# Kernel optimization log

Hardware: AMD Instinct MI355X
Metric: run time of the kernel (lower is better)

Reference implementation:

```python
import jax, jax.numpy as jnp
import numpy as np

B, N, D = 8, 512, 1024
E, H, TOP_K = 8, 8, 2
HD = D // H
EPS = 1e-5


def setup_inputs() -> dict:
    key = jax.random.key(0)
    ks = jax.random.split(key, 8)
    # kaiming_uniform with a=sqrt(5) over fan_in=N -> bound = sqrt(6/((1+5)*N)) = 1/sqrt(N)
    bound_w = 1.0 / np.sqrt(N)
    bound_lin = 1.0 / np.sqrt(D)
    return {
        "x": jax.random.normal(ks[0], (B, N, D), dtype=jnp.float32),
        "weight": jax.random.uniform(ks[1], (E, H, N, N), jnp.float32, -bound_w, bound_w),
        "bias": jnp.zeros((E, H, N), jnp.float32),
        "router_w": jax.random.uniform(ks[2], (E, D), jnp.float32, -bound_lin, bound_lin),
        "in_w": jax.random.uniform(ks[3], (D, D), jnp.float32, -bound_lin, bound_lin),
        "in_b": jax.random.uniform(ks[4], (D,), jnp.float32, -bound_lin, bound_lin),
        "out_w": jax.random.uniform(ks[5], (D, D), jnp.float32, -bound_lin, bound_lin),
        "out_b": jax.random.uniform(ks[6], (D,), jnp.float32, -bound_lin, bound_lin),
    }


def reference(x, weight, bias, router_w, in_w, in_b, out_w, out_b):
    # Router: mean-pool tokens, linear, softmax, top-k
    router_logits = x.mean(axis=1) @ router_w.T              # (B, E)
    router_probs = jax.nn.softmax(router_logits, axis=-1)
    top_w, top_i = jax.lax.top_k(router_probs, TOP_K)        # (B, K)
    top_w = top_w / top_w.sum(axis=-1, keepdims=True)

    # Input projection -> (B, H, hd, N), layer-norm over token axis N (no affine)
    xp = x @ in_w.T + in_b                                   # (B, N, D)
    xr = xp.reshape(B, N, H, HD).transpose(0, 2, 3, 1)       # (B, H, hd, N)
    mu = xr.mean(axis=-1, keepdims=True)
    var = xr.var(axis=-1, keepdims=True)
    xn = (xr - mu) * jax.lax.rsqrt(var + EPS)

    # Gather per-(batch, head, k) NxN expert matrices, row-softmax
    w = weight[top_i].transpose(0, 2, 1, 3, 4)               # (B, H, K, N, N)
    b = bias[top_i].transpose(0, 2, 1, 3)                    # (B, H, K, N)
    w_attn = jax.nn.softmax(w, axis=-1)

    # out[b,h,k,d,m] = sum_n xn[b,h,d,n] * w_attn[b,h,k,m,n]
    out = jnp.einsum('bhdn,bhkmn->bhkdm', xn, w_attn)
    out = out + b[:, :, :, None, :]                          # (B, H, K, hd, N)
    out = (out * top_w[:, None, :, None, None]).sum(axis=2)  # (B, H, hd, N)

    out = out.transpose(0, 3, 1, 2).reshape(B, N, D)         # (B, N, D)
    out = out @ out_w.T + out_b

    # Load-balancing aux loss
    top1 = top_i[:, 0]
    expert_mask = jax.nn.one_hot(top1, E, dtype=jnp.float32)
    aux = E * (router_probs.mean(axis=0) * expert_mask.mean(axis=0)).sum()
    return out, aux
```

## Files before the change

### kernel.cpp

```cpp
#include <hip/hip_runtime.h>
#include <hip/hip_bf16.h>

#define Bv 8
#define Nv 512
#define Dv 1024
#define Ev 8
#define Hv 8
#define HDv 128
#define EPSv 1e-5f

typedef __attribute__((ext_vector_type(8))) short short8;
typedef __attribute__((ext_vector_type(4))) float f32x4;

__device__ __forceinline__ unsigned short f2b(float f) {
    __hip_bfloat16 h = __float2bfloat16(f);
    return *reinterpret_cast<unsigned short*>(&h);
}
__device__ __forceinline__ float bf2f(unsigned int u) {
    union { unsigned int i; float f; } v; v.i = u << 16; return v.f;
}
__device__ __forceinline__ unsigned int blend2(unsigned int a, unsigned int b,
                                               float tw0, float tw1) {
    float lo = tw0 * bf2f(a & 0xffffu) + tw1 * bf2f(b & 0xffffu);
    float hi = tw0 * bf2f(a >> 16)     + tw1 * bf2f(b >> 16);
    return (unsigned int)f2b(lo) | ((unsigned int)f2b(hi) << 16);
}

__device__ __forceinline__ void gld16(const void* g, void* l) {
    __builtin_amdgcn_global_load_lds(
        (const __attribute__((address_space(1))) void*)(uintptr_t)(g),
        (__attribute__((address_space(3))) void*)(uintptr_t)(l), 16, 0, 0);
}

__global__ __launch_bounds__(256) void k_pre(const float* __restrict__ x,
                                             const float* __restrict__ weight,
                                             const float* __restrict__ w1,
                                             const float* __restrict__ w2,
                                             unsigned short* __restrict__ xb,
                                             float* __restrict__ part_x,
                                             unsigned short* __restrict__ wa,
                                             unsigned short* __restrict__ w1b,
                                             unsigned short* __restrict__ w2b) {
    int bid = blockIdx.x;
    int t = threadIdx.x;
    if (bid < 128) {
        int b = bid >> 4, c = bid & 15;
        const float* px = x + ((size_t)b * Nv + c * 32) * Dv + t * 4;
        unsigned short* qx = xb + ((size_t)b * Nv + c * 32) * Dv + t * 4;
        float4 s4 = make_float4(0.f, 0.f, 0.f, 0.f);
        #pragma unroll 8
        for (int r = 0; r < 32; ++r) {
            float4 v = *(const float4*)(px + (size_t)r * Dv);
            s4.x += v.x; s4.y += v.y; s4.z += v.z; s4.w += v.w;
            uint2 pk;
            pk.x = (unsigned)f2b(v.x) | ((unsigned)f2b(v.y) << 16);
            pk.y = (unsigned)f2b(v.z) | ((unsigned)f2b(v.w) << 16);
            *(uint2*)(qx + (size_t)r * Dv) = pk;
        }
        *(float4*)(part_x + ((size_t)(b * 16 + c)) * Dv + t * 4) = s4;
        return;
    }
    if (bid < 1152) {
        int lane = t & 63;
        int r0 = ((bid - 128) * 4 + (t >> 6)) * 8;
        const float* wp = weight + (size_t)r0 * Nv + lane * 4;
        float v[8][8];
        #pragma unroll
        for (int r = 0; r < 8; ++r) {
            float4 a = *(const float4*)(wp + (size_t)r * Nv);
            float4 b = *(const float4*)(wp + (size_t)r * Nv + 256);
            v[r][0] = a.x; v[r][1] = a.y; v[r][2] = a.z; v[r][3] = a.w;
            v[r][4] = b.x; v[r][5] = b.y; v[r][6] = b.z; v[r][7] = b.w;
        }
        float sm[8];
        #pragma unroll
        for (int r = 0; r < 8; ++r) {
            #pragma unroll
            for (int i = 0; i < 8; ++i) v[r][i] = __expf(v[r][i]);
            float s01 = v[r][0] + v[r][1], s23 = v[r][2] + v[r][3];
            float s45 = v[r][4] + v[r][5], s67 = v[r][6] + v[r][7];
            sm[r] = (s01 + s23) + (s45 + s67);
        }
        for (int off = 1; off < 64; off <<= 1) {
            #pragma unroll
            for (int r = 0; r < 8; ++r) sm[r] += __shfl_xor(sm[r], off);
        }
        unsigned short* wq = wa + (size_t)r0 * Nv + lane * 4;
        #pragma unroll
        for (int r = 0; r < 8; ++r) {
            float inv = 1.f / sm[r];
            uint2 p0, p1;
            p0.x = (unsigned)f2b(v[r][0] * inv) | ((unsigned)f2b(v[r][1] * inv) << 16);
            p0.y = (unsigned)f2b(v[r][2] * inv) | ((unsigned)f2b(v[r][3] * inv) << 16);
            p1.x = (unsigned)f2b(v[r][4] * inv) | ((unsigned)f2b(v[r][5] * inv) << 16);
            p1.y = (unsigned)f2b(v[r][6] * inv) | ((unsigned)f2b(v[r][7] * inv) << 16);
            *(uint2*)(wq + (size_t)r * Nv) = p0;
            *(uint2*)(wq + (size_t)r * Nv + 256) = p1;
        }
        return;
    }
    int base = (bid - 1152) * 2048;
    const float* src; unsigned short* dst;
    if (base < 1048576) { src = w1; dst = w1b; }
    else                { src = w2; dst = w2b; base -= 1048576; }
    float4 a = *(const float4*)(src + base + t * 4);
    float4 b = *(const float4*)(src + base + 1024 + t * 4);
    uint2 p0, p1;
    p0.x = (unsigned)f2b(a.x) | ((unsigned)f2b(a.y) << 16);
    p0.y = (unsigned)f2b(a.z) | ((unsigned)f2b(a.w) << 16);
    p1.x = (unsigned)f2b(b.x) | ((unsigned)f2b(b.y) << 16);
    p1.y = (unsigned)f2b(b.z) | ((unsigned)f2b(b.w) << 16);
    *(uint2*)(dst + base + t * 4) = p0;
    *(uint2*)(dst + base + 1024 + t * 4) = p1;
}

template <int MODE>
__global__ __launch_bounds__(256) void k_gemm(
    const unsigned short* __restrict__ A,
    const unsigned short* __restrict__ W,
    const float* __restrict__ bias,
    void* __restrict__ Cv,
    float2* __restrict__ part,
    const float* __restrict__ part_x,
    float* __restrict__ xmean,
    int M, int Nn, int K) {
    __shared__ __align__(16) unsigned short sA[3][128 * 64];
    __shared__ __align__(16) unsigned short sB[3][128 * 64];
    const int t = threadIdx.x;
    const int bn = blockIdx.x * 128;
    const int bm = blockIdx.y * 128;
    const int lane = t & 63;
    const int w = t >> 6, wm = w >> 1, wn = w & 1;
    const int fr = lane & 15, fq = lane >> 4;
    const int NT = K >> 6;
    f32x4 acc[4][4] = {};

#define STAGE(s, k0)                                                        \
    {                                                                       \
        _Pragma("unroll")                                                   \
        for (int i_ = 0; i_ < 4; ++i_) {                                    \
            int c_ = t + i_ * 256;                                          \
            int row_ = c_ >> 3, col_ = c_ & 7;                              \
            int cs_ = col_ ^ (row_ & 7);                                    \
            gld16(A + (size_t)(bm + row_) * K + (k0) + cs_ * 8, &sA[s][c_ * 8]); \
            gld16(W + (size_t)(bn + row_) * K + (k0) + cs_ * 8, &sB[s][c_ * 8]); \
        }                                                                   \
    }

    STAGE(0, 0);
    STAGE(1, 64);
    if (MODE == 2) {
        int blk = blockIdx.y * 8 + blockIdx.x;
        int o = blk * 32 + (t >> 3);
        int c2 = t & 7;
        int b2 = o >> 10, d2 = o & 1023;
        float S = part_x[((size_t)(b2 * 16 + c2)) * Dv + d2]
                + part_x[((size_t)(b2 * 16 + c2 + 8)) * Dv + d2];
        S += __shfl_xor(S, 1); S += __shfl_xor(S, 2); S += __shfl_xor(S, 4);
        if (c2 == 0) xmean[o] = S * (1.f / Nv);
    }
    for (int it = 0; it < NT; ++it) {
        if (it + 2 < NT) {
            STAGE((it + 2) % 3, (it + 2) * 64);
            asm volatile("s_waitcnt vmcnt(16)" ::: "memory");
        } else if (it + 1 < NT) {
            asm volatile("s_waitcnt vmcnt(8)" ::: "memory");
        } else {
            asm volatile("s_waitcnt vmcnt(0)" ::: "memory");
        }
        __builtin_amdgcn_s_barrier();
        const unsigned short* pA = sA[it % 3];
        const unsigned short* pB = sB[it % 3];
        #pragma unroll
        for (int kk = 0; kk < 2; ++kk) {
            short8 af[4], bv[4];
            #pragma unroll
            for (int i = 0; i < 4; ++i)
                af[i] = *(const short8*)&pA[(wm * 64 + i * 16 + fr) * 64 + (((kk << 2) + fq) ^ (fr & 7)) * 8];
            #pragma unroll
            for (int j = 0; j < 4; ++j)
                bv[j] = *(const short8*)&pB[(wn * 64 + j * 16 + fr) * 64 + (((kk << 2) + fq) ^ (fr & 7)) * 8];
            #pragma unroll
            for (int i = 0; i < 4; ++i)
                #pragma unroll
                for (int j = 0; j < 4; ++j)
                    acc[i][j] = __builtin_amdgcn_mfma_f32_16x16x32_bf16(af[i], bv[j], acc[i][j], 0, 0, 0);
        }
        __builtin_amdgcn_s_barrier();
    }
#undef STAGE
    if (MODE == 0) {
        #pragma unroll
        for (int j = 0; j < 4; ++j) {
            const int n = bn + wn * 64 + j * 16 + fr;
            const float bj = bias[n];
            #pragma unroll
            for (int i = 0; i < 4; ++i) {
                const int m0 = bm + wm * 64 + i * 16 + fq * 4;
                #pragma unroll
                for (int r = 0; r < 4; ++r)
                    ((float*)Cv)[(size_t)(m0 + r) * Nn + n] = acc[i][j][r] + bj;
            }
        }
    } else {
        unsigned short* sc = &sA[0][0];
        float2* red = (float2*)&sB[0][0];
        const int bB   = bm >> 9;
        const int tok0 = bm & 511;
        const int chunk = (bm >> 7) & 3;
        #pragma unroll
        for (int j = 0; j < 4; ++j) {
            const int col = wn * 64 + j * 16 + fr;
            const float bj = bias[bn + col];
            float s = 0.f, q = 0.f;
            #pragma unroll
            for (int i = 0; i < 4; ++i) {
                const int row0 = wm * 64 + i * 16 + fq * 4;
                #pragma unroll
                for (int r = 0; r < 4; r += 2) {
                    float v0 = acc[i][j][r] + bj;
                    float v1 = acc[i][j][r + 1] + bj;
                    s += v0 + v1;
                    q = fmaf(v0, v0, fmaf(v1, v1, q));
                    unsigned int pk = (unsigned int)f2b(v0) | ((unsigned int)f2b(v1) << 16);
                    *(unsigned int*)&sc[col * 136 + row0 + r] = pk;
                }
            }
            red[col * 8 + wm * 4 + fq] = make_float2(s, q);
        }
        __syncthreads();
        if (t < 128) {
            float S = 0.f, Q = 0.f;
            #pragma unroll
            for (int k = 0; k < 8; ++k) { float2 v = red[t * 8 + k]; S += v.x; Q += v.y; }
            part[((size_t)bB * Dv + bn + t) * 4 + chunk] = make_float2(S, Q);
        }
        unsigned short* dst = (unsigned short*)Cv;
        #pragma unroll
        for (int k = 0; k < 8; ++k) {
            const int c = t + k * 256;
            const int dl = c >> 4, tk = c & 15;
            uint4 v = *(const uint4*)&sc[dl * 136 + tk * 8];
            *(uint4*)&dst[((size_t)bB * Dv + bn + dl) * Nv + tok0 + tk * 8] = v;
        }
    }
}

__global__ __launch_bounds__(256) void k_mixg(
    const unsigned short* __restrict__ wa,
    const unsigned short* __restrict__ xpT,
    const float* __restrict__ bias,
    const float* __restrict__ xmean,
    const float* __restrict__ router_w,
    const float2* __restrict__ part,
    unsigned short* __restrict__ y,
    float* __restrict__ aux_out) {
    __shared__ __align__(16) unsigned short sA[2][128 * 64];
    __shared__ __align__(16) unsigned short sB[2][128 * 64];
    __shared__ float probs[Bv][Ev];
    __shared__ float twsh[Bv][2];
    __shared__ int   tsel[Bv][2];
    __shared__ int   top1s[Bv];
    const int t = threadIdx.x;
    const int bm = blockIdx.x * 128;
    const int bh = blockIdx.y;
    const int b = bh >> 3, h = bh & 7;

    {
        int pid = t >> 2, l = t & 3;
        int rb = pid >> 3, re = pid & 7;
        const float4* xm = (const float4*)(xmean + rb * Dv);
        const float4* rw = (const float4*)(router_w + re * Dv);
        float s = 0.f;
        #pragma unroll
        for (int j = 0; j < 64; ++j) {
            float4 aa = xm[l + j * 4], ww = rw[l + j * 4];
            s = fmaf(aa.x, ww.x, s); s = fmaf(aa.y, ww.y, s);
            s = fmaf(aa.z, ww.z, s); s = fmaf(aa.w, ww.w, s);
        }
        s += __shfl_xor(s, 1); s += __shfl_xor(s, 2);
        if (l == 0) probs[rb][re] = s;
    }
    __syncthreads();
    if (t < Bv) {
        int bb = t;
        float mx = -1e30f;
        for (int e2 = 0; e2 < Ev; ++e2) mx = fmaxf(mx, probs[bb][e2]);
        float sum = 0.f;
        for (int e2 = 0; e2 < Ev; ++e2) { float v = __expf(probs[bb][e2] - mx); probs[bb][e2] = v; sum += v; }
        float inv = 1.f / sum;
        for (int e2 = 0; e2 < Ev; ++e2) probs[bb][e2] *= inv;
        int i0 = 0; float p0 = probs[bb][0];
        for (int e2 = 1; e2 < Ev; ++e2) if (probs[bb][e2] > p0) { p0 = probs[bb][e2]; i0 = e2; }
        int i1 = -1; float p1 = -1.f;
        for (int e2 = 0; e2 < Ev; ++e2) if (e2 != i0 && probs[bb][e2] > p1) { p1 = probs[bb][e2]; i1 = e2; }
        float s2 = p0 + p1;
        tsel[bb][0] = i0; tsel[bb][1] = i1;
        twsh[bb][0] = p0 / s2; twsh[bb][1] = p1 / s2;
        top1s[bb] = i0;
    }
    __syncthreads();
    if (blockIdx.x == 0 && bh == 0 && t == 0) {
        float aux = 0.f;
        for (int e2 = 0; e2 < Ev; ++e2) {
            float pm = 0.f, mm = 0.f;
            for (int bb = 0; bb < Bv; ++bb) { pm += probs[bb][e2]; mm += (top1s[bb] == e2) ? 1.f : 0.f; }
            aux += (pm / Bv) * (mm / Bv);
        }
        *aux_out = aux * Ev;
    }
    const int e0 = tsel[b][0], e1 = tsel[b][1];
    const float tw0 = twsh[b][0], tw1 = twsh[b][1];

    const int lane = t & 63;
    const int w = t >> 6, wm = w >> 1, wn = w & 1;
    const int fr = lane & 15, fq = lane >> 4;

    float rstd_j[4], nmr_j[4];
    #pragma unroll
    for (int j = 0; j < 4; ++j) {
        const int dg = h * HDv + wn * 64 + j * 16 + fr;
        const float2* pp = part + ((size_t)b * Dv + dg) * 4;
        float S = 0.f, Q = 0.f;
        #pragma unroll
        for (int cc = 0; cc < 4; ++cc) { float2 v = pp[cc]; S += v.x; Q += v.y; }
        float mu = S * (1.f / Nv);
        float var = Q * (1.f / Nv) - mu * mu;
        float rs = rsqrtf(var + EPSv);
        rstd_j[j] = rs; nmr_j[j] = -mu * rs;
    }

    const unsigned short* A0 = wa + (size_t)(e0 * Hv + h) * Nv * Nv;
    const unsigned short* A1 = wa + (size_t)(e1 * Hv + h) * Nv * Nv;
    const unsigned short* Bb = xpT + ((size_t)b * Dv + h * HDv) * Nv;
    const int NT = Nv >> 6;
    f32x4 acc[4][4] = {};
    uint4 ra0[4], ra1[4];

#define BSTAGE(s, k0)                                                       \
    {                                                                       \
        _Pragma("unroll")                                                   \
        for (int i_ = 0; i_ < 4; ++i_) {                                    \
            int c_ = t + i_ * 256;                                          \
            int row_ = c_ >> 3, col_ = c_ & 7;                              \
            int cs_ = col_ ^ (row_ & 7);                                    \
            gld16(Bb + (size_t)row_ * Nv + (k0) + cs_ * 8, &sB[s][c_ * 8]); \
        }                                                                   \
    }
#define ALOAD(k0)                                                           \
    {                                                                       \
        _Pragma("unroll")                                                   \
        for (int i_ = 0; i_ < 4; ++i_) {                                    \
            int c_ = t + i_ * 256;                                          \
            int row_ = c_ >> 3, col_ = c_ & 7;                              \
            int cs_ = col_ ^ (row_ & 7);                                    \
            size_t off_ = (size_t)(bm + row_) * Nv + (k0) + cs_ * 8;        \
            ra0[i_] = *(const uint4*)&A0[off_];                             \
            ra1[i_] = *(const uint4*)&A1[off_];                             \
        }                                                                   \
    }

    BSTAGE(0, 0);
    ALOAD(0);
    for (int it = 0; it < NT; ++it) {
        if (it + 1 < NT) {
            BSTAGE((it + 1) & 1, (it + 1) * 64);
            asm volatile("s_waitcnt vmcnt(4)" ::: "memory");
        } else {
            asm volatile("s_waitcnt vmcnt(0)" ::: "memory");
        }
        #pragma unroll
        for (int i = 0; i < 4; ++i) {
            int c = t + i * 256;
            uint4 o;
            o.x = blend2(ra0[i].x, ra1[i].x, tw0, tw1);
            o.y = blend2(ra0[i].y, ra1[i].y, tw0, tw1);
            o.z = blend2(ra0[i].z, ra1[i].z, tw0, tw1);
            o.w = blend2(ra0[i].w, ra1[i].w, tw0, tw1);
            *(uint4*)&sA[it & 1][c * 8] = o;
        }
        if (it + 1 < NT) ALOAD((it + 1) * 64);
        asm volatile("s_waitcnt lgkmcnt(0)" ::: "memory");
        __builtin_amdgcn_s_barrier();
        const unsigned short* pA = sA[it & 1];
        const unsigned short* pB = sB[it & 1];
        #pragma unroll
        for (int kk = 0; kk < 2; ++kk) {
            short8 af[4], bv[4];
            #pragma unroll
            for (int i = 0; i < 4; ++i)
                af[i] = *(const short8*)&pA[(wm * 64 + i * 16 + fr) * 64 + (((kk << 2) + fq) ^ (fr & 7)) * 8];
            #pragma unroll
            for (int j = 0; j < 4; ++j)
                bv[j] = *(const short8*)&pB[(wn * 64 + j * 16 + fr) * 64 + (((kk << 2) + fq) ^ (fr & 7)) * 8];
            #pragma unroll
            for (int i = 0; i < 4; ++i)
                #pragma unroll
                for (int j = 0; j < 4; ++j)
                    acc[i][j] = __builtin_amdgcn_mfma_f32_16x16x32_bf16(af[i], bv[j], acc[i][j], 0, 0, 0);
        }
        __builtin_amdgcn_s_barrier();
    }
#undef BSTAGE
#undef ALOAD
    #pragma unroll
    for (int i = 0; i < 4; ++i) {
        #pragma unroll
        for (int r = 0; r < 4; ++r) {
            const int m = bm + wm * 64 + i * 16 + fq * 4 + r;
            const float br = tw0 * bias[(size_t)(e0 * Hv + h) * Nv + m]
                           + tw1 * bias[(size_t)(e1 * Hv + h) * Nv + m];
            #pragma unroll
            for (int j = 0; j < 4; ++j) {
                const int d = wn * 64 + j * 16 + fr;
                float v = fmaf(acc[i][j][r], rstd_j[j], nmr_j[j] + br);
                y[((size_t)b * Nv + m) * Dv + h * HDv + d] = f2b(v);
            }
        }
    }
}

extern "C" void kernel_launch(void* const* d_in, const int* in_sizes, int n_in,
                              void* d_out, int out_size, void* d_ws, size_t ws_size,
                              hipStream_t stream) {
    const float* x        = (const float*)d_in[0];
    const float* weight   = (const float*)d_in[1];
    const float* bias     = (const float*)d_in[2];
    const float* router_w = (const float*)d_in[3];
    const float* in_w     = (const float*)d_in[4];
    const float* in_b     = (const float*)d_in[5];
    const float* out_w    = (const float*)d_in[6];
    const float* out_b    = (const float*)d_in[7];
    float* out = (float*)d_out;

    if (ws_size < ((size_t)63 << 20)) return;

    char* wsb = (char*)d_ws;
    float*  xmean  = (float*)(wsb);
    float2* part   = (float2*)(wsb + (64 << 10));
    float*  part_x = (float*)(wsb + (512 << 10));
    unsigned short* in_wb  = (unsigned short*)(wsb + ((size_t)2 << 20));
    unsigned short* out_wb = (unsigned short*)(wsb + ((size_t)4 << 20));
    unsigned short* xb     = (unsigned short*)(wsb + ((size_t)8 << 20));
    unsigned short* xpT    = (unsigned short*)(wsb + ((size_t)16 << 20));
    unsigned short* wa     = (unsigned short*)(wsb + ((size_t)24 << 20));
    unsigned short* y = xb;

    k_pre<<<2176, 256, 0, stream>>>(x, weight, in_w, out_w, xb, part_x, wa, in_wb, out_wb);
    k_gemm<2><<<dim3(8, 32), 256, 0, stream>>>(xb, in_wb, in_b, xpT, part, part_x, xmean,
                                               Bv * Nv, Dv, Dv);
    k_mixg<<<dim3(4, 64), 256, 0, stream>>>(wa, xpT, bias, xmean, router_w, part, y,
                                            out + (size_t)Bv * Nv * Dv);
    k_gemm<0><<<dim3(8, 32), 256, 0, stream>>>(y, out_wb, out_b, out, nullptr, nullptr, nullptr,
                                               Bv * Nv, Dv, Dv);
}
```

Measured before the change: 75.50 us.

## Overlap expert-weight softmax and out_w conversion with the input-projection GEMM

The expert-weight softmax and the out_w bf16 conversion move out of the pre-kernel and into extra blocks of the first GEMM launch. Those memory-bound blocks can then fill CUs alongside the 256 GEMM tiles, and the pre-kernel shrinks to the x conversion plus the in_w cast. To fit occupancy, the first GEMM's LDS pipeline drops from triple to double buffering, which risks exposing load latency. The output GEMM becomes a separate non-templated kernel.

After: 77.03 us. +2.0%, slower.

```diff
diff --git a/kernel.cpp b/kernel.cpp
--- a/kernel.cpp
+++ b/kernel.cpp
@@ -32,15 +32,11 @@
         (__attribute__((address_space(3))) void*)(uintptr_t)(l), 16, 0, 0);
 }
 
-__global__ __launch_bounds__(256) void k_pre(const float* __restrict__ x,
-                                             const float* __restrict__ weight,
-                                             const float* __restrict__ w1,
-                                             const float* __restrict__ w2,
-                                             unsigned short* __restrict__ xb,
-                                             float* __restrict__ part_x,
-                                             unsigned short* __restrict__ wa,
-                                             unsigned short* __restrict__ w1b,
-                                             unsigned short* __restrict__ w2b) {
+__global__ __launch_bounds__(256) void k_preA(const float* __restrict__ x,
+                                              const float* __restrict__ w1,
+                                              unsigned short* __restrict__ xb,
+                                              float* __restrict__ part_x,
+                                              unsigned short* __restrict__ w1b) {
     int bid = blockIdx.x;
     int t = threadIdx.x;
     if (bid < 128) {
@@ -60,98 +56,108 @@
         *(float4*)(part_x + ((size_t)(b * 16 + c)) * Dv + t * 4) = s4;
         return;
     }
-    if (bid < 1152) {
-        int lane = t & 63;
-        int r0 = ((bid - 128) * 4 + (t >> 6)) * 8;
-        const float* wp = weight + (size_t)r0 * Nv + lane * 4;
-        float v[8][8];
-        #pragma unroll
-        for (int r = 0; r < 8; ++r) {
-            float4 a = *(const float4*)(wp + (size_t)r * Nv);
-            float4 b = *(const float4*)(wp + (size_t)r * Nv + 256);
-            v[r][0] = a.x; v[r][1] = a.y; v[r][2] = a.z; v[r][3] = a.w;
-            v[r][4] = b.x; v[r][5] = b.y; v[r][6] = b.z; v[r][7] = b.w;
-        }
-        float sm[8];
-        #pragma unroll
-        for (int r = 0; r < 8; ++r) {
-            #pragma unroll
-            for (int i = 0; i < 8; ++i) v[r][i] = __expf(v[r][i]);
-            float s01 = v[r][0] + v[r][1], s23 = v[r][2] + v[r][3];
-            float s45 = v[r][4] + v[r][5], s67 = v[r][6] + v[r][7];
-            sm[r] = (s01 + s23) + (s45 + s67);
-        }
-        for (int off = 1; off < 64; off <<= 1) {
-            #pragma unroll
-            for (int r = 0; r < 8; ++r) sm[r] += __shfl_xor(sm[r], off);
-        }
-        unsigned short* wq = wa + (size_t)r0 * Nv + lane * 4;
-        #pragma unroll
-        for (int r = 0; r < 8; ++r) {
-            float inv = 1.f / sm[r];
-            uint2 p0, p1;
-            p0.x = (unsigned)f2b(v[r][0] * inv) | ((unsigned)f2b(v[r][1] * inv) << 16);
-            p0.y = (unsigned)f2b(v[r][2] * inv) | ((unsigned)f2b(v[r][3] * inv) << 16);
-            p1.x = (unsigned)f2b(v[r][4] * inv) | ((unsigned)f2b(v[r][5] * inv) << 16);
-            p1.y = (unsigned)f2b(v[r][6] * inv) | ((unsigned)f2b(v[r][7] * inv) << 16);
-            *(uint2*)(wq + (size_t)r * Nv) = p0;
-            *(uint2*)(wq + (size_t)r * Nv + 256) = p1;
-        }
-        return;
-    }
-    int base = (bid - 1152) * 2048;
-    const float* src; unsigned short* dst;
-    if (base < 1048576) { src = w1; dst = w1b; }
-    else                { src = w2; dst = w2b; base -= 1048576; }
-    float4 a = *(const float4*)(src + base + t * 4);
-    float4 b = *(const float4*)(src + base + 1024 + t * 4);
-    uint2 p0, p1;
-    p0.x = (unsigned)f2b(a.x) | ((unsigned)f2b(a.y) << 16);
-    p0.y = (unsigned)f2b(a.z) | ((unsigned)f2b(a.w) << 16);
-    p1.x = (unsigned)f2b(b.x) | ((unsigned)f2b(b.y) << 16);
-    p1.y = (unsigned)f2b(b.z) | ((unsigned)f2b(b.w) << 16);
-    *(uint2*)(dst + base + t * 4) = p0;
-    *(uint2*)(dst + base + 1024 + t * 4) = p1;
-}
-
-template <int MODE>
-__global__ __launch_bounds__(256) void k_gemm(
+    int base = (bid - 128) * 8192;
+    #pragma unroll
+    for (int i = 0; i < 8; ++i) {
+        float4 a = *(const float4*)(w1 + base + i * 1024 + t * 4);
+        uint2 p;
+        p.x = (unsigned)f2b(a.x) | ((unsigned)f2b(a.y) << 16);
+        p.y = (unsigned)f2b(a.z) | ((unsigned)f2b(a.w) << 16);
+        *(uint2*)(w1b + base + i * 1024 + t * 4) = p;
+    }
+}
+
+__global__ __launch_bounds__(256) void k_g1s(
     const unsigned short* __restrict__ A,
     const unsigned short* __restrict__ W,
     const float* __restrict__ bias,
-    void* __restrict__ Cv,
+    unsigned short* __restrict__ Cv,
     float2* __restrict__ part,
     const float* __restrict__ part_x,
     float* __restrict__ xmean,
-    int M, int Nn, int K) {
-    __shared__ __align__(16) unsigned short sA[3][128 * 64];
-    __shared__ __align__(16) unsigned short sB[3][128 * 64];
+    const float* __restrict__ weight,
+    unsigned short* __restrict__ wa,
+    const float* __restrict__ w2,
+    unsigned short* __restrict__ w2b) {
+    __shared__ __align__(16) unsigned short sh[2][2][128 * 64];
+    const int bid = blockIdx.x;
     const int t = threadIdx.x;
-    const int bn = blockIdx.x * 128;
-    const int bm = blockIdx.y * 128;
+
+    if (bid >= 256) {
+        if (bid < 1280) {
+            int lane = t & 63;
+            int r0 = (((bid - 256) * 4) + (t >> 6)) * 8;
+            const float* wp = weight + (size_t)r0 * Nv + lane * 4;
+            float v[8][8];
+            #pragma unroll
+            for (int r = 0; r < 8; ++r) {
+                float4 a = *(const float4*)(wp + (size_t)r * Nv);
+                float4 b = *(const float4*)(wp + (size_t)r * Nv + 256);
+                v[r][0] = a.x; v[r][1] = a.y; v[r][2] = a.z; v[r][3] = a.w;
+                v[r][4] = b.x; v[r][5] = b.y; v[r][6] = b.z; v[r][7] = b.w;
+            }
+            float sm[8];
+            #pragma unroll
+            for (int r = 0; r < 8; ++r) {
+                #pragma unroll
+                for (int i = 0; i < 8; ++i) v[r][i] = __expf(v[r][i]);
+                float s01 = v[r][0] + v[r][1], s23 = v[r][2] + v[r][3];
+                float s45 = v[r][4] + v[r][5], s67 = v[r][6] + v[r][7];
+                sm[r] = (s01 + s23) + (s45 + s67);
+            }
+            for (int off = 1; off < 64; off <<= 1) {
+                #pragma unroll
+                for (int r = 0; r < 8; ++r) sm[r] += __shfl_xor(sm[r], off);
+            }
+            unsigned short* wq = wa + (size_t)r0 * Nv + lane * 4;
+            #pragma unroll
+            for (int r = 0; r < 8; ++r) {
+                float inv = 1.f / sm[r];
+                uint2 p0, p1;
+                p0.x = (unsigned)f2b(v[r][0] * inv) | ((unsigned)f2b(v[r][1] * inv) << 16);
+                p0.y = (unsigned)f2b(v[r][2] * inv) | ((unsigned)f2b(v[r][3] * inv) << 16);
+                p1.x = (unsigned)f2b(v[r][4] * inv) | ((unsigned)f2b(v[r][5] * inv) << 16);
+                p1.y = (unsigned)f2b(v[r][6] * inv) | ((unsigned)f2b(v[r][7] * inv) << 16);
+                *(uint2*)(wq + (size_t)r * Nv) = p0;
+                *(uint2*)(wq + (size_t)r * Nv + 256) = p1;
+            }
+            return;
+        }
+        int base = (bid - 1280) * 8192;
+        #pragma unroll
+        for (int i = 0; i < 8; ++i) {
+            float4 a = *(const float4*)(w2 + base + i * 1024 + t * 4);
+            uint2 p;
+            p.x = (unsigned)f2b(a.x) | ((unsigned)f2b(a.y) << 16);
+            p.y = (unsigned)f2b(a.z) | ((unsigned)f2b(a.w) << 16);
+            *(uint2*)(w2b + base + i * 1024 + t * 4) = p;
+        }
+        return;
+    }
+
+    const int bn = (bid & 7) * 128;
+    const int bm = (bid >> 3) * 128;
     const int lane = t & 63;
     const int w = t >> 6, wm = w >> 1, wn = w & 1;
     const int fr = lane & 15, fq = lane >> 4;
-    const int NT = K >> 6;
+    const int K = Dv, NT = 16;
     f32x4 acc[4][4] = {};
 
-#define STAGE(s, k0)                                                        \
+#define STAGE2(s, k0)                                                       \
     {                                                                       \
         _Pragma("unroll")                                                   \
         for (int i_ = 0; i_ < 4; ++i_) {                                    \
             int c_ = t + i_ * 256;                                          \
             int row_ = c_ >> 3, col_ = c_ & 7;                              \
             int cs_ = col_ ^ (row_ & 7);                                    \
-            gld16(A + (size_t)(bm + row_) * K + (k0) + cs_ * 8, &sA[s][c_ * 8]); \
-            gld16(W + (size_t)(bn + row_) * K + (k0) + cs_ * 8, &sB[s][c_ * 8]); \
+            gld16(A + (size_t)(bm + row_) * K + (k0) + cs_ * 8, &sh[0][s][c_ * 8]); \
+            gld16(W + (size_t)(bn + row_) * K + (k0) + cs_ * 8, &sh[1][s][c_ * 8]); \
         }                                                                   \
     }
 
-    STAGE(0, 0);
-    STAGE(1, 64);
-    if (MODE == 2) {
-        int blk = blockIdx.y * 8 + blockIdx.x;
-        int o = blk * 32 + (t >> 3);
+    STAGE2(0, 0);
+    {
+        int o = bid * 32 + (t >> 3);
         int c2 = t & 7;
         int b2 = o >> 10, d2 = o & 1023;
         float S = part_x[((size_t)(b2 * 16 + c2)) * Dv + d2]
@@ -160,17 +166,15 @@
         if (c2 == 0) xmean[o] = S * (1.f / Nv);
     }
     for (int it = 0; it < NT; ++it) {
-        if (it + 2 < NT) {
-            STAGE((it + 2) % 3, (it + 2) * 64);
-            asm volatile("s_waitcnt vmcnt(16)" ::: "memory");
-        } else if (it + 1 < NT) {
+        if (it + 1 < NT) {
+            STAGE2((it + 1) & 1, (it + 1) * 64);
             asm volatile("s_waitcnt vmcnt(8)" ::: "memory");
         } else {
             asm volatile("s_waitcnt vmcnt(0)" ::: "memory");
         }
         __builtin_amdgcn_s_barrier();
-        const unsigned short* pA = sA[it % 3];
-        const unsigned short* pB = sB[it % 3];
+        const unsigned short* pA = sh[0][it & 1];
+        const unsigned short* pB = sh[1][it & 1];
         #pragma unroll
         for (int kk = 0; kk < 2; ++kk) {
             short8 af[4], bv[4];
@@ -188,61 +192,46 @@
         }
         __builtin_amdgcn_s_barrier();
     }
-#undef STAGE
-    if (MODE == 0) {
-        #pragma unroll
-        for (int j = 0; j < 4; ++j) {
-            const int n = bn + wn * 64 + j * 16 + fr;
-            const float bj = bias[n];
-            #pragma unroll
-            for (int i = 0; i < 4; ++i) {
-                const int m0 = bm + wm * 64 + i * 16 + fq * 4;
-                #pragma unroll
-                for (int r = 0; r < 4; ++r)
-                    ((float*)Cv)[(size_t)(m0 + r) * Nn + n] = acc[i][j][r] + bj;
+#undef STAGE2
+
+    unsigned short* sc = &sh[0][0][0];
+    float2* red = (float2*)((char*)&sh[0][0][0] + 36864);
+    const int bB   = bm >> 9;
+    const int tok0 = bm & 511;
+    const int chunk = (bm >> 7) & 3;
+    #pragma unroll
+    for (int j = 0; j < 4; ++j) {
+        const int col = wn * 64 + j * 16 + fr;
+        const float bj = bias[bn + col];
+        float s = 0.f, q = 0.f;
+        #pragma unroll
+        for (int i = 0; i < 4; ++i) {
+            const int row0 = wm * 64 + i * 16 + fq * 4;
+            #pragma unroll
+            for (int r = 0; r < 4; r += 2) {
+                float v0 = acc[i][j][r] + bj;
+                float v1 = acc[i][j][r + 1] + bj;
+                s += v0 + v1;
+                q = fmaf(v0, v0, fmaf(v1, v1, q));
+                unsigned int pk = (unsigned int)f2b(v0) | ((unsigned int)f2b(v1) << 16);
+                *(unsigned int*)&sc[col * 136 + row0 + r] = pk;
             }
         }
-    } else {
-        unsigned short* sc = &sA[0][0];
-        float2* red = (float2*)&sB[0][0];
-        const int bB   = bm >> 9;
-        const int tok0 = bm & 511;
-        const int chunk = (bm >> 7) & 3;
-        #pragma unroll
-        for (int j = 0; j < 4; ++j) {
-            const int col = wn * 64 + j * 16 + fr;
-            const float bj = bias[bn + col];
-            float s = 0.f, q = 0.f;
-            #pragma unroll
-            for (int i = 0; i < 4; ++i) {
-                const int row0 = wm * 64 + i * 16 + fq * 4;
-                #pragma unroll
-                for (int r = 0; r < 4; r += 2) {
-                    float v0 = acc[i][j][r] + bj;
-                    float v1 = acc[i][j][r + 1] + bj;
-                    s += v0 + v1;
-                    q = fmaf(v0, v0, fmaf(v1, v1, q));
-                    unsigned int pk = (unsigned int)f2b(v0) | ((unsigned int)f2b(v1) << 16);
-                    *(unsigned int*)&sc[col * 136 + row0 + r] = pk;
-                }
-            }
-            red[col * 8 + wm * 4 + fq] = make_float2(s, q);
-        }
-        __syncthreads();
-        if (t < 128) {
-            float S = 0.f, Q = 0.f;
-            #pragma unroll
-            for (int k = 0; k < 8; ++k) { float2 v = red[t * 8 + k]; S += v.x; Q += v.y; }
-            part[((size_t)bB * Dv + bn + t) * 4 + chunk] = make_float2(S, Q);
-        }
-        unsigned short* dst = (unsigned short*)Cv;
-        #pragma unroll
-        for (int k = 0; k < 8; ++k) {
-            const int c = t + k * 256;
-            const int dl = c >> 4, tk = c & 15;
-            uint4 v = *(const uint4*)&sc[dl * 136 + tk * 8];
-            *(uint4*)&dst[((size_t)bB * Dv + bn + dl) * Nv + tok0 + tk * 8] = v;
-        }
+        red[col * 8 + wm * 4 + fq] = make_float2(s, q);
+    }
+    __syncthreads();
+    if (t < 128) {
+        float S = 0.f, Q = 0.f;
+        #pragma unroll
+        for (int k = 0; k < 8; ++k) { float2 v = red[t * 8 + k]; S += v.x; Q += v.y; }
+        part[((size_t)bB * Dv + bn + t) * 4 + chunk] = make_float2(S, Q);
+    }
+    #pragma unroll
+    for (int k = 0; k < 8; ++k) {
+        const int c = t + k * 256;
+        const int dl = c >> 4, tk = c & 15;
+        uint4 v = *(const uint4*)&sc[dl * 136 + tk * 8];
+        *(uint4*)&Cv[((size_t)bB * Dv + bn + dl) * Nv + tok0 + tk * 8] = v;
     }
 }
 
@@ -420,6 +409,80 @@
     }
 }
 
+__global__ __launch_bounds__(256) void k_gemm0(
+    const unsigned short* __restrict__ A,
+    const unsigned short* __restrict__ W,
+    const float* __restrict__ bias,
+    float* __restrict__ C) {
+    __shared__ __align__(16) unsigned short sA[3][128 * 64];
+    __shared__ __align__(16) unsigned short sB[3][128 * 64];
+    const int t = threadIdx.x;
+    const int bn = blockIdx.x * 128;
+    const int bm = blockIdx.y * 128;
+    const int lane = t & 63;
+    const int w = t >> 6, wm = w >> 1, wn = w & 1;
+    const int fr = lane & 15, fq = lane >> 4;
+    const int K = Dv, NT = 16, Nn = Dv;
+    f32x4 acc[4][4] = {};
+
+#define STAGE(s, k0)                                                        \
+    {                                                                       \
+        _Pragma("unroll")                                                   \
+        for (int i_ = 0; i_ < 4; ++i_) {                                    \
+            int c_ = t + i_ * 256;                                          \
+            int row_ = c_ >> 3, col_ = c_ & 7;                              \
+            int cs_ = col_ ^ (row_ & 7);                                    \
+            gld16(A + (size_t)(bm + row_) * K + (k0) + cs_ * 8, &sA[s][c_ * 8]); \
+            gld16(W + (size_t)(bn + row_) * K + (k0) + cs_ * 8, &sB[s][c_ * 8]); \
+        }                                                                   \
+    }
+
+    STAGE(0, 0);
+    STAGE(1, 64);
+    for (int it = 0; it < NT; ++it) {
+        if (it + 2 < NT) {
+            STAGE((it + 2) % 3, (it + 2) * 64);
+            asm volatile("s_waitcnt vmcnt(16)" ::: "memory");
+        } else if (it + 1 < NT) {
+            asm volatile("s_waitcnt vmcnt(8)" ::: "memory");
+        } else {
+            asm volatile("s_waitcnt vmcnt(0)" ::: "memory");
+        }
+        __builtin_amdgcn_s_barrier();
+        const unsigned short* pA = sA[it % 3];
+        const unsigned short* pB = sB[it % 3];
+        #pragma unroll
+        for (int kk = 0; kk < 2; ++kk) {
+            short8 af[4], bv[4];
+            #pragma unroll
+            for (int i = 0; i < 4; ++i)
+                af[i] = *(const short8*)&pA[(wm * 64 + i * 16 + fr) * 64 + (((kk << 2) + fq) ^ (fr & 7)) * 8];
+            #pragma unroll
+            for (int j = 0; j < 4; ++j)
+                bv[j] = *(const short8*)&pB[(wn * 64 + j * 16 + fr) * 64 + (((kk << 2) + fq) ^ (fr & 7)) * 8];
+            #pragma unroll
+            for (int i = 0; i < 4; ++i)
+                #pragma unroll
+                for (int j = 0; j < 4; ++j)
+                    acc[i][j] = __builtin_amdgcn_mfma_f32_16x16x32_bf16(af[i], bv[j], acc[i][j], 0, 0, 0);
+        }
+        __builtin_amdgcn_s_barrier();
+    }
+#undef STAGE
+    #pragma unroll
+    for (int j = 0; j < 4; ++j) {
+        const int n = bn + wn * 64 + j * 16 + fr;
+        const float bj = bias[n];
+        #pragma unroll
+        for (int i = 0; i < 4; ++i) {
+            const int m0 = bm + wm * 64 + i * 16 + fq * 4;
+            #pragma unroll
+            for (int r = 0; r < 4; ++r)
+                C[(size_t)(m0 + r) * Nn + n] = acc[i][j][r] + bj;
+        }
+    }
+}
+
 extern "C" void kernel_launch(void* const* d_in, const int* in_sizes, int n_in,
                               void* d_out, int out_size, void* d_ws, size_t ws_size,
                               hipStream_t stream) {
@@ -446,11 +509,10 @@
     unsigned short* wa     = (unsigned short*)(wsb + ((size_t)24 << 20));
     unsigned short* y = xb;
 
-    k_pre<<<2176, 256, 0, stream>>>(x, weight, in_w, out_w, xb, part_x, wa, in_wb, out_wb);
-    k_gemm<2><<<dim3(8, 32), 256, 0, stream>>>(xb, in_wb, in_b, xpT, part, part_x, xmean,
-                                               Bv * Nv, Dv, Dv);
+    k_preA<<<256, 256, 0, stream>>>(x, in_w, xb, part_x, in_wb);
+    k_g1s<<<1408, 256, 0, stream>>>(xb, in_wb, in_b, xpT, part, part_x, xmean,
+                                    weight, wa, out_w, out_wb);
     k_mixg<<<dim3(4, 64), 256, 0, stream>>>(wa, xpT, bias, xmean, router_w, part, y,
                                             out + (size_t)Bv * Nv * Dv);
-    k_gemm<0><<<dim3(8, 32), 256, 0, stream>>>(y, out_wb, out_b, out, nullptr, nullptr, nullptr,
-                                               Bv * Nv, Dv, Dv);
-}
+    k_gemm0<<<dim3(8, 32), 256, 0, stream>>>(y, out_wb, out_b, out);
+}
```
